# Performance work log

Measured on AMD Instinct MI355X. Metric: run time of the kernel, lower is better.

The kernel has to match this reference:

```python
import jax, jax.numpy as jnp
import numpy as np

N, D, E, OUT = 50000, 256, 320000, 1

def setup_inputs() -> dict:
    key = jax.random.key(0)
    k1, k2, k3, k4, k5, k6 = jax.random.split(key, 6)
    z = jax.random.normal(k1, (N, D), dtype=jnp.float32)
    edge_index = jax.random.randint(k2, (2, E), 0, N, dtype=jnp.int64)
    # xavier_normal for fc1: std = sqrt(2/(fan_in+fan_out)) = sqrt(2/(2D+D))
    w1 = jax.random.normal(k3, (D, 2 * D), dtype=jnp.float32) * np.sqrt(2.0 / (3 * D))
    b1 = jnp.zeros((D,), dtype=jnp.float32)
    w2 = jax.random.normal(k4, (OUT, D), dtype=jnp.float32) * np.sqrt(2.0 / (D + OUT))
    b2 = jnp.zeros((OUT,), dtype=jnp.float32)
    return {"z": z, "edge_index": edge_index, "w1": w1, "b1": b1, "w2": w2, "b2": b2}

def reference(z, edge_index, w1, b1, w2, b2):
    x1 = z[edge_index[0]]                     # [E, D]
    x2 = z[edge_index[1]]                     # [E, D]
    x = jnp.concatenate([x1, x2], axis=1)     # [E, 2D]
    h = jax.nn.relu(x @ w1.T + b1)            # [E, D]
    return h @ w2.T + b2                      # [E, OUT]
```

## Files before the change

### kernel.cpp

```cpp
#include <hip/hip_runtime.h>
#include <hip/hip_bf16.h>

#define D 256
#define TWOD 512
#define BM 128
#define BK 32

typedef __attribute__((ext_vector_type(8))) __bf16 bf16x8;
typedef __attribute__((ext_vector_type(4))) float f32x4;
typedef __attribute__((ext_vector_type(8))) unsigned short ushort8;

using as1_u32 = __attribute__((address_space(1))) const unsigned int;
using as3_u32 = __attribute__((address_space(3))) unsigned int;

__device__ __forceinline__ void gload_lds16(const void* g, void* l) {
    __builtin_amdgcn_global_load_lds((as1_u32*)g, (as3_u32*)l, 16, 0, 0);
}

__device__ __forceinline__ float bf2f(unsigned short u) {
    unsigned int x = ((unsigned int)u) << 16;
    return __uint_as_float(x);
}
__device__ __forceinline__ unsigned short f2bf_bits(float f) {
    unsigned int x = __float_as_uint(f);
    unsigned int r = (x + 0x7fffu + ((x >> 16) & 1u)) >> 16;
    return (unsigned short)r;
}

__global__ __launch_bounds__(256) void wt_conv_kernel(
    const float* __restrict__ w1, unsigned short* __restrict__ Wt)
{
    const int s = blockIdx.x * 256 + threadIdx.x;
    const int j = s >> 9;
    const int kk = s & 511;
    const float v = w1[s];
    const int dst = (kk < D) ? (j * D + kk) : ((D + j) * D + (kk - D));
    Wt[dst] = f2bf_bits(v);
}

__global__ __launch_bounds__(256, 3) void node_proj_mfma(
    const float* __restrict__ z, const unsigned short* __restrict__ Wt,
    unsigned short* __restrict__ C, int M, int Mblocks)
{
    __shared__ __align__(16) float          Abuf[2][BM * BK];
    __shared__ __align__(16) unsigned short Bbuf[2][BM * BK];

    const int bid    = blockIdx.x;
    const int rowblk = (bid >> 5) * 8 + (bid & 7);
    if (rowblk >= Mblocks) return;
    const int m0 = rowblk * BM;
    const int cb = ((bid >> 3) & 3) * BM;

    const int t    = threadIdx.x;
    const int lane = t & 63;
    const int w    = t >> 6;

    const int r16 = lane & 15;
    const int g   = lane >> 4;

    const int wm = (w >> 1) * 64;
    const int wn = (w & 1) * 64;

    f32x4 acc[4][4];
    #pragma unroll
    for (int mt = 0; mt < 4; ++mt)
        #pragma unroll
        for (int nt = 0; nt < 4; ++nt)
            acc[mt][nt] = (f32x4){0.f, 0.f, 0.f, 0.f};

    auto stage = [&](int buf, int k0) {
        #pragma unroll
        for (int i = 0; i < 4; ++i) {
            const int c = i * 256 + t;
            const int r = c >> 3;
            const int q = c & 7;
            const int col = ((q ^ (r & 7)) << 2);
            const int row = min(m0 + r, M - 1);
            const float* gsrc = z + (size_t)row * D + k0 + col;
            float* ldst = &Abuf[buf][(size_t)(i * 256 + w * 64) * 4];
            gload_lds16(gsrc, ldst);
        }
        #pragma unroll
        for (int i = 0; i < 2; ++i) {
            const int c = i * 256 + t;
            const int r = c >> 2;
            const int q = c & 3;
            const int sb = (r ^ (r >> 2)) & 3;
            const int col = ((q ^ sb) << 3);
            const unsigned short* gsrc = Wt + (size_t)(cb + r) * D + k0 + col;
            unsigned short* ldst = &Bbuf[buf][(size_t)(i * 256 + w * 64) * 8];
            gload_lds16(gsrc, ldst);
        }
    };

    stage(0, 0);
    __syncthreads();

    int buf = 0;
    #pragma unroll
    for (int kt = 0; kt < 8; ++kt) {
        if (kt < 7) stage(buf ^ 1, (kt + 1) * BK);

        bf16x8 b[4];
        #pragma unroll
        for (int nt = 0; nt < 4; ++nt) {
            const int rl = wn + nt * 16 + r16;
            const int sb = (rl ^ (rl >> 2)) & 3;
            const ushort8 bu = *(const ushort8*)&Bbuf[buf][rl * 32 + ((g ^ sb) << 3)];
            b[nt] = __builtin_bit_cast(bf16x8, bu);
        }
        bf16x8 a[4];
        #pragma unroll
        for (int mt = 0; mt < 4; ++mt) {
            const int rl = wm + mt * 16 + r16;
            const int s = rl & 7;
            const f32x4 f0 = *(const f32x4*)&Abuf[buf][rl * 32 + (((2 * g) ^ s) << 2)];
            const f32x4 f1 = *(const f32x4*)&Abuf[buf][rl * 32 + (((2 * g + 1) ^ s) << 2)];
            bf16x8 tt;
            tt[0] = (__bf16)f0[0]; tt[1] = (__bf16)f0[1];
            tt[2] = (__bf16)f0[2]; tt[3] = (__bf16)f0[3];
            tt[4] = (__bf16)f1[0]; tt[5] = (__bf16)f1[1];
            tt[6] = (__bf16)f1[2]; tt[7] = (__bf16)f1[3];
            a[mt] = tt;
        }

        #pragma unroll
        for (int nt = 0; nt < 4; ++nt)
            #pragma unroll
            for (int mt = 0; mt < 4; ++mt)
                acc[mt][nt] = __builtin_amdgcn_mfma_f32_16x16x32_bf16(
                    b[nt], a[mt], acc[mt][nt], 0, 0, 0);

        __syncthreads();
        buf ^= 1;
    }

    #pragma unroll
    for (int mt = 0; mt < 4; ++mt) {
        const int row = m0 + wm + mt * 16 + r16;
        if (row < M) {
            #pragma unroll
            for (int nt = 0; nt < 4; ++nt) {
                const int col = cb + wn + nt * 16 + g * 4;
                ushort4 pk;
                pk.x = f2bf_bits(acc[mt][nt][0]);
                pk.y = f2bf_bits(acc[mt][nt][1]);
                pk.z = f2bf_bits(acc[mt][nt][2]);
                pk.w = f2bf_bits(acc[mt][nt][3]);
                *(ushort4*)(C + (size_t)row * TWOD + col) = pk;
            }
        }
    }
}

__global__ __launch_bounds__(256) void edge_kernel(
    const int* __restrict__ ei, const unsigned short* __restrict__ C,
    const float* __restrict__ b1, const float* __restrict__ w2,
    const float* __restrict__ b2, float* __restrict__ out, int E)
{
    const int h   = threadIdx.x & 31;
    const int gid = (blockIdx.x * blockDim.x + threadIdx.x) >> 5;
    const int ng  = (gridDim.x * blockDim.x) >> 5;
    const int j0  = h * 8;

    const float4 w2a = *(const float4*)(w2 + j0);
    const float4 w2b = *(const float4*)(w2 + j0 + 4);
    const float4 b1a = *(const float4*)(b1 + j0);
    const float4 b1b = *(const float4*)(b1 + j0 + 4);
    const float  b2s = b2[0];

    auto dot8 = [&](const ushort8& ua, const ushort8& ub) -> float {
        float s;
        s  = fmaxf(bf2f(ua[0]) + bf2f(ub[0]) + b1a.x, 0.f) * w2a.x;
        s += fmaxf(bf2f(ua[1]) + bf2f(ub[1]) + b1a.y, 0.f) * w2a.y;
        s += fmaxf(bf2f(ua[2]) + bf2f(ub[2]) + b1a.z, 0.f) * w2a.z;
        s += fmaxf(bf2f(ua[3]) + bf2f(ub[3]) + b1a.w, 0.f) * w2a.w;
        s += fmaxf(bf2f(ua[4]) + bf2f(ub[4]) + b1b.x, 0.f) * w2b.x;
        s += fmaxf(bf2f(ua[5]) + bf2f(ub[5]) + b1b.y, 0.f) * w2b.y;
        s += fmaxf(bf2f(ua[6]) + bf2f(ub[6]) + b1b.z, 0.f) * w2b.z;
        s += fmaxf(bf2f(ua[7]) + bf2f(ub[7]) + b1b.w, 0.f) * w2b.w;
        return s;
    };

    int e = gid;
    for (; e + ng < E; e += 2 * ng) {
        const int e1 = e + ng;
        const int u0 = ei[e],  v0 = ei[E + e];
        const int u1 = ei[e1], v1 = ei[E + e1];

        const ushort8 ua0 = *(const ushort8*)(C + (size_t)u0 * TWOD + j0);
        const ushort8 ub0 = *(const ushort8*)(C + (size_t)v0 * TWOD + D + j0);
        const ushort8 ua1 = *(const ushort8*)(C + (size_t)u1 * TWOD + j0);
        const ushort8 ub1 = *(const ushort8*)(C + (size_t)v1 * TWOD + D + j0);

        float s0 = dot8(ua0, ub0);
        float s1 = dot8(ua1, ub1);

        #pragma unroll
        for (int off = 16; off; off >>= 1) {
            s0 += __shfl_xor(s0, off);
            s1 += __shfl_xor(s1, off);
        }

        if (h == 0) {
            out[e]  = s0 + b2s;
            out[e1] = s1 + b2s;
        }
    }
    if (e < E) {
        const int u = ei[e], v = ei[E + e];
        const ushort8 ua = *(const ushort8*)(C + (size_t)u * TWOD + j0);
        const ushort8 ub = *(const ushort8*)(C + (size_t)v * TWOD + D + j0);
        float s = dot8(ua, ub);
        #pragma unroll
        for (int off = 16; off; off >>= 1)
            s += __shfl_xor(s, off);
        if (h == 0) out[e] = s + b2s;
    }
}

extern "C" void kernel_launch(void* const* d_in, const int* in_sizes, int n_in,
                              void* d_out, int out_size, void* d_ws, size_t ws_size,
                              hipStream_t stream) {
    const float* z  = (const float*)d_in[0];
    const int*   ei = (const int*)d_in[1];
    const float* w1 = (const float*)d_in[2];
    const float* b1 = (const float*)d_in[3];
    const float* w2 = (const float*)d_in[4];
    const float* b2 = (const float*)d_in[5];
    float* out = (float*)d_out;

    const int M = in_sizes[0] / D;
    const int E = in_sizes[1] / 2;

    unsigned short* C  = (unsigned short*)d_ws;
    unsigned short* Wt = (unsigned short*)d_out;

    wt_conv_kernel<<<512, 256, 0, stream>>>(w1, Wt);

    const int Mblocks = (M + BM - 1) / BM;
    const int stripes = (Mblocks + 7) / 8;
    node_proj_mfma<<<stripes * 32, 256, 0, stream>>>(z, Wt, C, M, Mblocks);

    edge_kernel<<<4096, 256, 0, stream>>>(ei, C, b1, w2, b2, out, E);
}
```

Baseline: 91.27 us.

## Triple-buffer GEMM staging with manual waitcnt and widen edge-kernel unroll to four

The node projection GEMM moves from a double-buffered LDS pipeline to a triple-buffered one, staging two k-tiles ahead. Each k-step now uses a manual vmcnt wait and a single barrier instead of two syncs, and the MFMA block runs at raised wave priority. Occupancy is lowered to two blocks per SM to fit the larger LDS footprint. The edge kernel processes four edges per iteration instead of two to keep more gathers in flight, at the cost of extra registers.

Result: slower. 93.38 us (+2.3%).

```diff
diff --git a/kernel.cpp b/kernel.cpp
--- a/kernel.cpp
+++ b/kernel.cpp
@@ -38,12 +38,12 @@
     Wt[dst] = f2bf_bits(v);
 }
 
-__global__ __launch_bounds__(256, 3) void node_proj_mfma(
+__global__ __launch_bounds__(256, 2) void node_proj_mfma(
     const float* __restrict__ z, const unsigned short* __restrict__ Wt,
     unsigned short* __restrict__ C, int M, int Mblocks)
 {
-    __shared__ __align__(16) float          Abuf[2][BM * BK];
-    __shared__ __align__(16) unsigned short Bbuf[2][BM * BK];
+    __shared__ __align__(16) float          Abuf[3][BM * BK];
+    __shared__ __align__(16) unsigned short Bbuf[3][BM * BK];
 
     const int bid    = blockIdx.x;
     const int rowblk = (bid >> 5) * 8 + (bid & 7);
@@ -93,14 +93,7 @@
         }
     };
 
-    stage(0, 0);
-    __syncthreads();
-
-    int buf = 0;
-    #pragma unroll
-    for (int kt = 0; kt < 8; ++kt) {
-        if (kt < 7) stage(buf ^ 1, (kt + 1) * BK);
-
+    auto compute = [&](int buf) {
         bf16x8 b[4];
         #pragma unroll
         for (int nt = 0; nt < 4; ++nt) {
@@ -124,16 +117,29 @@
             a[mt] = tt;
         }
 
+        __builtin_amdgcn_s_setprio(1);
         #pragma unroll
         for (int nt = 0; nt < 4; ++nt)
             #pragma unroll
             for (int mt = 0; mt < 4; ++mt)
                 acc[mt][nt] = __builtin_amdgcn_mfma_f32_16x16x32_bf16(
                     b[nt], a[mt], acc[mt][nt], 0, 0, 0);
-
-        __syncthreads();
-        buf ^= 1;
-    }
+        __builtin_amdgcn_s_setprio(0);
+    };
+
+    stage(0, 0);
+    stage(1, BK);
+
+    #pragma unroll
+    for (int kt = 0; kt < 7; ++kt) {
+        asm volatile("s_waitcnt vmcnt(6)" ::: "memory");
+        asm volatile("s_barrier" ::: "memory");
+        if (kt + 2 < 8) stage((kt + 2) % 3, (kt + 2) * BK);
+        compute(kt % 3);
+    }
+    asm volatile("s_waitcnt vmcnt(0)" ::: "memory");
+    asm volatile("s_barrier" ::: "memory");
+    compute(7 % 3);
 
     #pragma unroll
     for (int mt = 0; mt < 4; ++mt) {
@@ -183,31 +189,43 @@
     };
 
     int e = gid;
-    for (; e + ng < E; e += 2 * ng) {
-        const int e1 = e + ng;
+    for (; e + 3 * ng < E; e += 4 * ng) {
+        const int e1 = e + ng, e2 = e + 2 * ng, e3 = e + 3 * ng;
         const int u0 = ei[e],  v0 = ei[E + e];
         const int u1 = ei[e1], v1 = ei[E + e1];
+        const int u2 = ei[e2], v2 = ei[E + e2];
+        const int u3 = ei[e3], v3 = ei[E + e3];
 
         const ushort8 ua0 = *(const ushort8*)(C + (size_t)u0 * TWOD + j0);
         const ushort8 ub0 = *(const ushort8*)(C + (size_t)v0 * TWOD + D + j0);
         const ushort8 ua1 = *(const ushort8*)(C + (size_t)u1 * TWOD + j0);
         const ushort8 ub1 = *(const ushort8*)(C + (size_t)v1 * TWOD + D + j0);
+        const ushort8 ua2 = *(const ushort8*)(C + (size_t)u2 * TWOD + j0);
+        const ushort8 ub2 = *(const ushort8*)(C + (size_t)v2 * TWOD + D + j0);
+        const ushort8 ua3 = *(const ushort8*)(C + (size_t)u3 * TWOD + j0);
+        const ushort8 ub3 = *(const ushort8*)(C + (size_t)v3 * TWOD + D + j0);
 
         float s0 = dot8(ua0, ub0);
         float s1 = dot8(ua1, ub1);
+        float s2 = dot8(ua2, ub2);
+        float s3 = dot8(ua3, ub3);
 
         #pragma unroll
         for (int off = 16; off; off >>= 1) {
             s0 += __shfl_xor(s0, off);
             s1 += __shfl_xor(s1, off);
+            s2 += __shfl_xor(s2, off);
+            s3 += __shfl_xor(s3, off);
         }
 
         if (h == 0) {
             out[e]  = s0 + b2s;
             out[e1] = s1 + b2s;
-        }
-    }
-    if (e < E) {
+            out[e2] = s2 + b2s;
+            out[e3] = s3 + b2s;
+        }
+    }
+    for (; e < E; e += ng) {
         const int u = ei[e], v = ei[E + e];
         const ushort8 ua = *(const ushort8*)(C + (size_t)u * TWOD + j0);
         const ushort8 ub = *(const ushort8*)(C + (size_t)v * TWOD + D + j0);
```

## Group edges by source node via counting sort and pre-pack weights for direct MFMA loads

Applied to the files above, without the earlier changes.

Adds a histogram, scan and scatter pass that buckets edges by source node. A new grouped edge kernel then loads each source row's projection once and reuses it for all of that node's edges. The weight matrix is pre-packed into an MFMA fragment layout so the projection GEMM reads B fragments straight from global memory, dropping the B LDS staging and raising the occupancy bound to 4. It also adds s_setprio around the MFMA block. The cost is several extra launches, atomics, a single-block serial scan, and scattered output writes, in exchange for fewer redundant gathers.

After: 188.3 us. 106% more time.

```diff
diff --git a/kernel.cpp b/kernel.cpp
--- a/kernel.cpp
+++ b/kernel.cpp
@@ -28,22 +28,25 @@
 }
 
 __global__ __launch_bounds__(256) void wt_conv_kernel(
-    const float* __restrict__ w1, unsigned short* __restrict__ Wt)
+    const float* __restrict__ w1, unsigned short* __restrict__ WtP)
 {
     const int s = blockIdx.x * 256 + threadIdx.x;
-    const int j = s >> 9;
-    const int kk = s & 511;
+    const int o = s >> 9;
+    const int i = s & 511;
     const float v = w1[s];
-    const int dst = (kk < D) ? (j * D + kk) : ((D + j) * D + (kk - D));
-    Wt[dst] = f2bf_bits(v);
-}
-
-__global__ __launch_bounds__(256, 3) void node_proj_mfma(
-    const float* __restrict__ z, const unsigned short* __restrict__ Wt,
+    const int jj = (i < D) ? o : (D + o);
+    const int k  = (i < D) ? i : (i - D);
+    const int c16 = jj >> 4, r = jj & 15;
+    const int kblk = k >> 5, kin = k & 31;
+    const int g = kin >> 3, kj = kin & 7;
+    WtP[(size_t)((c16 * 8 + kblk) * 512 + (r + 16 * g) * 8 + kj)] = f2bf_bits(v);
+}
+
+__global__ __launch_bounds__(256, 4) void node_proj_mfma(
+    const float* __restrict__ z, const unsigned short* __restrict__ WtP,
     unsigned short* __restrict__ C, int M, int Mblocks)
 {
-    __shared__ __align__(16) float          Abuf[2][BM * BK];
-    __shared__ __align__(16) unsigned short Bbuf[2][BM * BK];
+    __shared__ __align__(16) float Abuf[2][BM * BK];
 
     const int bid    = blockIdx.x;
     const int rowblk = (bid >> 5) * 8 + (bid & 7);
@@ -60,6 +63,7 @@
 
     const int wm = (w >> 1) * 64;
     const int wn = (w & 1) * 64;
+    const int c16b = (cb + wn) >> 4;
 
     f32x4 acc[4][4];
     #pragma unroll
@@ -68,7 +72,7 @@
         for (int nt = 0; nt < 4; ++nt)
             acc[mt][nt] = (f32x4){0.f, 0.f, 0.f, 0.f};
 
-    auto stage = [&](int buf, int k0) {
+    auto stageA = [&](int buf, int k0) {
         #pragma unroll
         for (int i = 0; i < 4; ++i) {
             const int c = i * 256 + t;
@@ -80,33 +84,21 @@
             float* ldst = &Abuf[buf][(size_t)(i * 256 + w * 64) * 4];
             gload_lds16(gsrc, ldst);
         }
-        #pragma unroll
-        for (int i = 0; i < 2; ++i) {
-            const int c = i * 256 + t;
-            const int r = c >> 2;
-            const int q = c & 3;
-            const int sb = (r ^ (r >> 2)) & 3;
-            const int col = ((q ^ sb) << 3);
-            const unsigned short* gsrc = Wt + (size_t)(cb + r) * D + k0 + col;
-            unsigned short* ldst = &Bbuf[buf][(size_t)(i * 256 + w * 64) * 8];
-            gload_lds16(gsrc, ldst);
-        }
     };
 
-    stage(0, 0);
+    stageA(0, 0);
     __syncthreads();
 
     int buf = 0;
     #pragma unroll
     for (int kt = 0; kt < 8; ++kt) {
-        if (kt < 7) stage(buf ^ 1, (kt + 1) * BK);
+        if (kt < 7) stageA(buf ^ 1, (kt + 1) * BK);
 
         bf16x8 b[4];
         #pragma unroll
         for (int nt = 0; nt < 4; ++nt) {
-            const int rl = wn + nt * 16 + r16;
-            const int sb = (rl ^ (rl >> 2)) & 3;
-            const ushort8 bu = *(const ushort8*)&Bbuf[buf][rl * 32 + ((g ^ sb) << 3)];
+            const ushort8 bu = *(const ushort8*)(
+                WtP + (size_t)(((c16b + nt) * 8 + kt) * 512 + lane * 8));
             b[nt] = __builtin_bit_cast(bf16x8, bu);
         }
         bf16x8 a[4];
@@ -124,12 +116,14 @@
             a[mt] = tt;
         }
 
+        __builtin_amdgcn_s_setprio(1);
         #pragma unroll
         for (int nt = 0; nt < 4; ++nt)
             #pragma unroll
             for (int mt = 0; mt < 4; ++mt)
                 acc[mt][nt] = __builtin_amdgcn_mfma_f32_16x16x32_bf16(
                     b[nt], a[mt], acc[mt][nt], 0, 0, 0);
+        __builtin_amdgcn_s_setprio(0);
 
         __syncthreads();
         buf ^= 1;
@@ -153,6 +147,103 @@
     }
 }
 
+__global__ __launch_bounds__(256) void hist_kernel(
+    const int* __restrict__ ei, int* __restrict__ counts, int E)
+{
+    const int e = blockIdx.x * 256 + threadIdx.x;
+    if (e < E) atomicAdd(&counts[ei[e]], 1);
+}
+
+__global__ __launch_bounds__(1024) void scan_kernel(
+    const int* __restrict__ counts, int* __restrict__ offsets, int N)
+{
+    __shared__ int ps[1024];
+    const int t = threadIdx.x;
+    const int chunk = (N + 1023) / 1024;
+    const int lo = t * chunk;
+    const int hi = min(lo + chunk, N);
+    int s = 0;
+    for (int i = lo; i < hi; ++i) s += counts[i];
+    ps[t] = s;
+    __syncthreads();
+    for (int off = 1; off < 1024; off <<= 1) {
+        int v = (t >= off) ? ps[t - off] : 0;
+        __syncthreads();
+        ps[t] += v;
+        __syncthreads();
+    }
+    int run = (t == 0) ? 0 : ps[t - 1];
+    for (int i = lo; i < hi; ++i) { offsets[i] = run; run += counts[i]; }
+    if (t == 1023) offsets[N] = run;
+}
+
+__global__ __launch_bounds__(256) void scatter_kernel(
+    const int* __restrict__ ei, int* __restrict__ cursor,
+    int2* __restrict__ payload, int E)
+{
+    const int e = blockIdx.x * 256 + threadIdx.x;
+    if (e < E) {
+        const int u = ei[e];
+        const int pos = atomicAdd(&cursor[u], 1);
+        payload[pos] = make_int2(ei[E + e], e);
+    }
+}
+
+__global__ __launch_bounds__(256) void edge_grouped_kernel(
+    const int* __restrict__ offsets, const int2* __restrict__ payload,
+    const unsigned short* __restrict__ C, const float* __restrict__ b1,
+    const float* __restrict__ w2, const float* __restrict__ b2,
+    float* __restrict__ out, int N)
+{
+    const int h = threadIdx.x & 31;
+    const int u = (blockIdx.x * 256 + threadIdx.x) >> 5;
+    if (u >= N) return;
+    const int start = offsets[u];
+    const int end   = offsets[u + 1];
+    if (start == end) return;
+    const int j0 = h * 8;
+
+    const ushort8 ua = *(const ushort8*)(C + (size_t)u * TWOD + j0);
+    float af[8], wl[8];
+    #pragma unroll
+    for (int j = 0; j < 8; ++j) {
+        af[j] = bf2f(ua[j]) + b1[j0 + j];
+        wl[j] = w2[j0 + j];
+    }
+    const float b2s = b2[0];
+    const unsigned short* Cb = C + D;
+
+    auto edot = [&](int v) -> float {
+        const ushort8 ub = *(const ushort8*)(Cb + (size_t)v * TWOD + j0);
+        float s = 0.f;
+        #pragma unroll
+        for (int j = 0; j < 8; ++j)
+            s += fmaxf(af[j] + bf2f(ub[j]), 0.f) * wl[j];
+        return s;
+    };
+
+    int p = start;
+    for (; p + 2 <= end; p += 2) {
+        const int2 ve0 = payload[p];
+        const int2 ve1 = payload[p + 1];
+        float s0 = edot(ve0.x);
+        float s1 = edot(ve1.x);
+        #pragma unroll
+        for (int off = 16; off; off >>= 1) {
+            s0 += __shfl_xor(s0, off);
+            s1 += __shfl_xor(s1, off);
+        }
+        if (h == 0) { out[ve0.y] = s0 + b2s; out[ve1.y] = s1 + b2s; }
+    }
+    if (p < end) {
+        const int2 ve = payload[p];
+        float s = edot(ve.x);
+        #pragma unroll
+        for (int off = 16; off; off >>= 1) s += __shfl_xor(s, off);
+        if (h == 0) out[ve.y] = s + b2s;
+    }
+}
+
 __global__ __launch_bounds__(256) void edge_kernel(
     const int* __restrict__ ei, const unsigned short* __restrict__ C,
     const float* __restrict__ b1, const float* __restrict__ w2,
@@ -182,32 +273,7 @@
         return s;
     };
 
-    int e = gid;
-    for (; e + ng < E; e += 2 * ng) {
-        const int e1 = e + ng;
-        const int u0 = ei[e],  v0 = ei[E + e];
-        const int u1 = ei[e1], v1 = ei[E + e1];
-
-        const ushort8 ua0 = *(const ushort8*)(C + (size_t)u0 * TWOD + j0);
-        const ushort8 ub0 = *(const ushort8*)(C + (size_t)v0 * TWOD + D + j0);
-        const ushort8 ua1 = *(const ushort8*)(C + (size_t)u1 * TWOD + j0);
-        const ushort8 ub1 = *(const ushort8*)(C + (size_t)v1 * TWOD + D + j0);
-
-        float s0 = dot8(ua0, ub0);
-        float s1 = dot8(ua1, ub1);
-
-        #pragma unroll
-        for (int off = 16; off; off >>= 1) {
-            s0 += __shfl_xor(s0, off);
-            s1 += __shfl_xor(s1, off);
-        }
-
-        if (h == 0) {
-            out[e]  = s0 + b2s;
-            out[e1] = s1 + b2s;
-        }
-    }
-    if (e < E) {
+    for (int e = gid; e < E; e += ng) {
         const int u = ei[e], v = ei[E + e];
         const ushort8 ua = *(const ushort8*)(C + (size_t)u * TWOD + j0);
         const ushort8 ub = *(const ushort8*)(C + (size_t)v * TWOD + D + j0);
@@ -233,14 +299,31 @@
     const int M = in_sizes[0] / D;
     const int E = in_sizes[1] / 2;
 
-    unsigned short* C  = (unsigned short*)d_ws;
-    unsigned short* Wt = (unsigned short*)d_out;
-
-    wt_conv_kernel<<<512, 256, 0, stream>>>(w1, Wt);
+    unsigned short* C = (unsigned short*)d_ws;
+    size_t off = ((size_t)M * TWOD * 2 + 255) & ~(size_t)255;
+    int*  counts  = (int*)((char*)d_ws + off); off += (((size_t)M * 4 + 255) & ~(size_t)255);
+    int*  offsets = (int*)((char*)d_ws + off); off += (((size_t)(M + 1) * 4 + 255) & ~(size_t)255);
+    int*  cursor  = (int*)((char*)d_ws + off); off += (((size_t)M * 4 + 255) & ~(size_t)255);
+    int2* payload = (int2*)((char*)d_ws + off); off += (size_t)E * 8;
+    const bool use_sort = (off <= ws_size);
+
+    unsigned short* WtP = (unsigned short*)d_out;
+
+    wt_conv_kernel<<<512, 256, 0, stream>>>(w1, WtP);
 
     const int Mblocks = (M + BM - 1) / BM;
     const int stripes = (Mblocks + 7) / 8;
-    node_proj_mfma<<<stripes * 32, 256, 0, stream>>>(z, Wt, C, M, Mblocks);
-
-    edge_kernel<<<4096, 256, 0, stream>>>(ei, C, b1, w2, b2, out, E);
-}
+    node_proj_mfma<<<stripes * 32, 256, 0, stream>>>(z, WtP, C, M, Mblocks);
+
+    if (use_sort) {
+        hipMemsetAsync(counts, 0, (size_t)M * 4, stream);
+        hist_kernel<<<(E + 255) / 256, 256, 0, stream>>>(ei, counts, E);
+        scan_kernel<<<1, 1024, 0, stream>>>(counts, offsets, M);
+        hipMemcpyAsync(cursor, offsets, (size_t)M * 4, hipMemcpyDeviceToDevice, stream);
+        scatter_kernel<<<(E + 255) / 256, 256, 0, stream>>>(ei, cursor, payload, E);
+        edge_grouped_kernel<<<(M * 32 + 255) / 256, 256, 0, stream>>>(
+            offsets, payload, C, b1, w2, b2, out, M);
+    } else {
+        edge_kernel<<<4096, 256, 0, stream>>>(ei, C, b1, w2, b2, out, E);
+    }
+}
```
